# Optimization experiments

Hardware: AMD Instinct MI355X
Metric: run time of the kernel (lower is better)

The kernel has to match this reference:

```python
import jax, jax.numpy as jnp
import numpy as np

WINDOW = 16  # window_size from init_kwargs


def sigmoid_cutoff(x):
    # max(min(1.2*sigmoid(x) - 0.1, 1), 0)
    return jnp.clip(1.2 * jax.nn.sigmoid(x) - 0.1, 0.0, 1.0)


def setup_inputs() -> dict:
    key = jax.random.key(0)
    k1, k2, k3 = jax.random.split(key, 3)
    B, S, H = 8, 2048, 1024
    x = jax.random.normal(k1, (B, S, H), dtype=jnp.float32)
    # Dense kernels (glorot-ish scale), x_layer has no bias, y_layer has bias
    Wx = jax.random.normal(k2, (H, H), dtype=jnp.float32) * (1.0 / np.sqrt(H))
    Wy = jax.random.normal(k3, (H, 2 * H), dtype=jnp.float32) * (1.0 / np.sqrt(H))
    by = jnp.zeros((2 * H,), dtype=jnp.float32)
    return {"x": x, "Wx": Wx, "Wy": Wy, "by": by}


def reference(x, Wx, Wy, by):
    B, S, H = x.shape
    # left-pad sequence with window_size-1 zeros, then project once (x_layer)
    xp = jnp.pad(x, ((0, 0), (WINDOW - 1, 0), (0, 0)))
    proj = jnp.einsum('bsh,hd->bsd', xp, Wx)  # [B, S+W-1, H]

    def step(state, i):
        # inputs[:, i:S+i] in the original loop
        inp = jax.lax.dynamic_slice_in_dim(proj, i, S, axis=1)  # [B,S,H]
        ns = jnp.einsum('bsh,hd->bsd', state, Wy) + by          # [B,S,2H]
        # reshape [B,S,2,H]: channel 0 = candidate, channel 1 = gate
        cand, gate_logits = jnp.split(ns, 2, axis=-1)
        gate = sigmoid_cutoff(gate_logits)
        new_state = jax.nn.relu(gate * (inp + cand) + (1.0 - gate) * state)
        return new_state, None

    state0 = jnp.zeros_like(x)
    state, _ = jax.lax.scan(step, state0, jnp.arange(WINDOW))
    return state
```

## Files before the change

### kernel.cpp

```cpp
#include <hip/hip_runtime.h>

#define H 1024
#define SEQ 2048
#define MROWS 16384
#define KD 1024
#define NTK 16
#define EPW 72

typedef _Float16 f16;
typedef _Float16 f16x8 __attribute__((ext_vector_type(8)));
typedef float f32x4 __attribute__((ext_vector_type(4)));

__device__ __forceinline__ float gate_fn(float x) {
    float s = 1.0f / (1.0f + __expf(-x));
    return fminf(fmaxf(1.2f * s - 0.1f, 0.0f), 1.0f);
}

__device__ __forceinline__ void gload_lds16(const void* g, void* lds) {
    __builtin_amdgcn_global_load_lds(
        (const __attribute__((address_space(1))) unsigned int*)g,
        (__attribute__((address_space(3))) unsigned int*)lds, 16, 0, 0);
}

__global__ void k_f32_to_f16(const float* __restrict__ in, f16* __restrict__ out) {
    size_t i = ((size_t)blockIdx.x * blockDim.x + threadIdx.x) * 8;
    float4 v0 = *(const float4*)(in + i);
    float4 v1 = *(const float4*)(in + i + 4);
    f16x8 o;
    o[0] = (f16)v0.x; o[1] = (f16)v0.y; o[2] = (f16)v0.z; o[3] = (f16)v0.w;
    o[4] = (f16)v1.x; o[5] = (f16)v1.y; o[6] = (f16)v1.z; o[7] = (f16)v1.w;
    *(f16x8*)(out + i) = o;
}

__global__ void k_transpose_f16(const float* __restrict__ Wsrc, f16* __restrict__ WT,
                                int K, int N) {
    __shared__ float tile[32][33];
    int n0 = blockIdx.x * 32, k0 = blockIdx.y * 32;
    for (int i = threadIdx.y; i < 32; i += 8)
        tile[i][threadIdx.x] = Wsrc[(size_t)(k0 + i) * N + n0 + threadIdx.x];
    __syncthreads();
    for (int i = threadIdx.y; i < 32; i += 8)
        WT[(size_t)(n0 + i) * K + k0 + threadIdx.x] = (f16)tile[threadIdx.x][i];
}

__global__ __launch_bounds__(256) void k_proj_gemm(const f16* __restrict__ A,
                                                   const f16* __restrict__ BT,
                                                   f16* __restrict__ P16) {
    __shared__ alignas(16) f16 Alds[128 * 32];
    __shared__ alignas(16) f16 Blds[128 * 32];
    const int tid = threadIdx.x;
    const int lane = tid & 63, wid = tid >> 6;
    const int l15 = lane & 15, l4 = lane >> 4;
    const int bm = blockIdx.x, bn = blockIdx.y;

    const f16* gA[2]; const f16* gB[2];
    char* ldsA[2]; char* ldsB[2];
#pragma unroll
    for (int it = 0; it < 2; ++it) {
        int c = it * 4 + wid;
        int row = c * 16 + (lane >> 2);
        int kch = (lane & 3) ^ ((row >> 1) & 3);
        gA[it] = A + (size_t)(bm * 128 + row) * KD + kch * 8;
        gB[it] = BT + (size_t)(bn * 128 + row) * KD + kch * 8;
        ldsA[it] = (char*)Alds + c * 1024;
        ldsB[it] = (char*)Blds + c * 1024;
    }

    int offA[2], offB[8];
#pragma unroll
    for (int m = 0; m < 2; ++m) {
        int row = wid * 32 + m * 16 + l15;
        offA[m] = row * 64 + ((l4 ^ ((row >> 1) & 3)) << 4);
    }
#pragma unroll
    for (int n = 0; n < 8; ++n) {
        int row = n * 16 + l15;
        offB[n] = row * 64 + ((l4 ^ ((row >> 1) & 3)) << 4);
    }

    f32x4 acc[2][8] = {};

    for (int kt = 0; kt < KD / 32; ++kt) {
        __syncthreads();
#pragma unroll
        for (int it = 0; it < 2; ++it) {
            gload_lds16(gA[it], ldsA[it]);
            gload_lds16(gB[it], ldsB[it]);
            gA[it] += 32; gB[it] += 32;
        }
        __syncthreads();
        f16x8 a[2], b[8];
#pragma unroll
        for (int m = 0; m < 2; ++m) a[m] = *(const f16x8*)((const char*)Alds + offA[m]);
#pragma unroll
        for (int n = 0; n < 8; ++n) b[n] = *(const f16x8*)((const char*)Blds + offB[n]);
#pragma unroll
        for (int n = 0; n < 8; ++n)
#pragma unroll
            for (int m = 0; m < 2; ++m)
                acc[m][n] = __builtin_amdgcn_mfma_f32_16x16x32_f16(a[m], b[n], acc[m][n], 0, 0, 0);
    }

#pragma unroll
    for (int m = 0; m < 2; ++m)
#pragma unroll
        for (int n = 0; n < 8; ++n) {
            int col = bn * 128 + n * 16 + l15;
#pragma unroll
            for (int r = 0; r < 4; ++r) {
                int row = bm * 128 + wid * 32 + m * 16 + l4 * 4 + r;
                P16[(size_t)row * H + col] = (f16)acc[m][n][r];
            }
        }
}

__global__ void k_step0(const f16* __restrict__ P16, const float* __restrict__ by,
                        f16* __restrict__ S16) {
    size_t idx = ((size_t)blockIdx.x * blockDim.x + threadIdx.x) * 8;
    int row = (int)(idx >> 10);
    int d = (int)(idx & 1023);
    int s = row & (SEQ - 1);
    f16x8 p = {};
    if (s >= 15) p = *(const f16x8*)(P16 + (size_t)(row - 15) * H + d);
    float4 byc0 = *(const float4*)(by + d);
    float4 byc1 = *(const float4*)(by + d + 4);
    float4 byg0 = *(const float4*)(by + H + d);
    float4 byg1 = *(const float4*)(by + H + d + 4);
    f16x8 sv;
#pragma unroll
    for (int j = 0; j < 8; ++j) {
        float byc = (j < 4) ? ((const float*)&byc0)[j] : ((const float*)&byc1)[j - 4];
        float byg = (j < 4) ? ((const float*)&byg0)[j] : ((const float*)&byg1)[j - 4];
        float g = gate_fn(byg);
        float v = fmaxf(g * ((float)p[j] + byc), 0.f);
        sv[j] = (f16)v;
    }
    *(f16x8*)(S16 + idx) = sv;
}

__global__ __launch_bounds__(512) void k_step_gemm256(const f16* __restrict__ A,
                                                      const f16* __restrict__ BT,
                                                      const f16* __restrict__ P16,
                                                      const float* __restrict__ by,
                                                      float* __restrict__ Out,
                                                      f16* __restrict__ Snext,
                                                      int stepi) {
    __shared__ alignas(16) char lds[131072];
    const int tid = threadIdx.x;
    const int lane = tid & 63, w = tid >> 6;
    const int l15 = lane & 15, l4 = lane >> 4;
    const int wr = w >> 2, wc = w & 3;

    const int orig = blockIdx.x;
    const int wg = (orig & 7) * 64 + (orig >> 3);
    const int bm = wg >> 3, cbn = wg & 7;

    const int r0 = w * 16 + (lane >> 2), r1 = r0 + 128;
    const int slot = (lane & 3) ^ ((r0 >> 1) & 3);
    const char* pA0 = (const char*)A + ((size_t)(bm * 256 + r0) * KD + slot * 8) * 2;
    const char* pA1 = (const char*)A + ((size_t)(bm * 256 + r1) * KD + slot * 8) * 2;
    const int gB0 = ((r0 >> 5) & 1) * H + cbn * 128 + (r0 >> 6) * 32 + (r0 & 31);
    const int gB1 = ((r1 >> 5) & 1) * H + cbn * 128 + (r1 >> 6) * 32 + (r1 & 31);
    const char* pB0 = (const char*)BT + ((size_t)gB0 * KD + slot * 8) * 2;
    const char* pB1 = (const char*)BT + ((size_t)gB1 * KD + slot * 8) * 2;
    const int dst = w * 1024 + lane * 16;

#define STAGE(bp) do { \
        gload_lds16(pA0,       (bp) + dst); \
        gload_lds16(pA1,       (bp) + 8192 + dst); \
        gload_lds16(pA0 + 64,  (bp) + 16384 + dst); \
        gload_lds16(pA1 + 64,  (bp) + 16384 + 8192 + dst); \
        gload_lds16(pB0,       (bp) + 32768 + dst); \
        gload_lds16(pB1,       (bp) + 32768 + 8192 + dst); \
        gload_lds16(pB0 + 64,  (bp) + 49152 + dst); \
        gload_lds16(pB1 + 64,  (bp) + 49152 + 8192 + dst); \
        pA0 += 128; pA1 += 128; pB0 += 128; pB1 += 128; } while (0)

    const int sx = (l4 ^ ((l15 >> 1) & 3)) << 4;
    int offA[8], offB[4];
#pragma unroll
    for (int m = 0; m < 8; ++m) offA[m] = (wr * 128 + m * 16 + l15) * 64 + sx;
#pragma unroll
    for (int n = 0; n < 4; ++n) offB[n] = 32768 + (wc * 64 + n * 16 + l15) * 64 + sx;

    f32x4 acc[8][4] = {};

    char* cb = lds;
    char* nx = lds + 65536;

    STAGE(cb);
    __syncthreads();

    for (int t = 0; t < NTK; ++t) {
        if (t + 1 < NTK) STAGE(nx);
#pragma unroll
        for (int kh = 0; kh < 2; ++kh) {
            f16x8 a[8], b[4];
#pragma unroll
            for (int m = 0; m < 8; ++m) a[m] = *(const f16x8*)(cb + kh * 16384 + offA[m]);
#pragma unroll
            for (int n = 0; n < 4; ++n) b[n] = *(const f16x8*)(cb + kh * 16384 + offB[n]);
            __builtin_amdgcn_s_setprio(1);
#pragma unroll
            for (int m = 0; m < 8; ++m)
#pragma unroll
                for (int n = 0; n < 4; ++n)
                    acc[m][n] = __builtin_amdgcn_mfma_f32_16x16x32_f16(a[m], b[n], acc[m][n], 0, 0, 0);
            __builtin_amdgcn_s_setprio(0);
        }
        __syncthreads();
        char* tmp = cb; cb = nx; nx = tmp;
    }
#undef STAGE

    const bool last = (stepi == 15);
    f16* Cand = (f16*)lds;
    f16* Gate = (f16*)(lds + 256 * EPW * 2);
#pragma unroll
    for (int rnd = 0; rnd < 2; ++rnd) {
#pragma unroll
        for (int m = 0; m < 8; ++m)
#pragma unroll
            for (int r4 = 0; r4 < 4; ++r4) {
                int row = wr * 128 + m * 16 + l4 * 4 + r4;
                int cr = wc * 16 + l15;
                Cand[row * EPW + cr] = (f16)acc[m][rnd][r4];
                Gate[row * EPW + cr] = (f16)acc[m][rnd + 2][r4];
            }
        __syncthreads();
        const int g = tid & 7;
        const int rb = tid >> 3;
        const int ctile = (g >> 1) * 32 + rnd * 16 + (g & 1) * 8;
        const int d = cbn * 128 + ctile;
        const int cr0 = g * 8;
        float4 byc0 = *(const float4*)(by + d);
        float4 byc1 = *(const float4*)(by + d + 4);
        float4 byg0 = *(const float4*)(by + H + d);
        float4 byg1 = *(const float4*)(by + H + d + 4);
#pragma unroll
        for (int p = 0; p < 4; ++p) {
            int row = p * 64 + rb;
            int grow = bm * 256 + row;
            int s = grow & (SEQ - 1);
            f16x8 c8 = *(const f16x8*)(Cand + row * EPW + cr0);
            f16x8 g8 = *(const f16x8*)(Gate + row * EPW + cr0);
            f16x8 p8 = {};
            if (s >= 15 - stepi)
                p8 = *(const f16x8*)(P16 + (size_t)(grow + stepi - 15) * H + d);
            f16x8 s8 = *(const f16x8*)(A + (size_t)grow * H + d);
            f16x8 o8; float ov[8];
#pragma unroll
            for (int j = 0; j < 8; ++j) {
                float byc = (j < 4) ? ((const float*)&byc0)[j] : ((const float*)&byc1)[j - 4];
                float byg = (j < 4) ? ((const float*)&byg0)[j] : ((const float*)&byg1)[j - 4];
                float cand = (float)c8[j] + byc;
                float gg = gate_fn((float)g8[j] + byg);
                float v = fmaxf(gg * ((float)p8[j] + cand) + (1.f - gg) * (float)s8[j], 0.f);
                o8[j] = (f16)v; ov[j] = v;
            }
            if (!last) {
                *(f16x8*)(Snext + (size_t)grow * H + d) = o8;
            } else {
                *(float4*)(Out + (size_t)grow * H + d) = make_float4(ov[0], ov[1], ov[2], ov[3]);
                *(float4*)(Out + (size_t)grow * H + d + 4) = make_float4(ov[4], ov[5], ov[6], ov[7]);
            }
        }
        __syncthreads();
    }
}

extern "C" void kernel_launch(void* const* d_in, const int* in_sizes, int n_in,
                              void* d_out, int out_size, void* d_ws, size_t ws_size,
                              hipStream_t stream) {
    (void)in_sizes; (void)n_in; (void)out_size; (void)ws_size;
    const float* x  = (const float*)d_in[0];
    const float* Wx = (const float*)d_in[1];
    const float* Wy = (const float*)d_in[2];
    const float* by = (const float*)d_in[3];
    float* out = (float*)d_out;

    char* ws = (char*)d_ws;
    const size_t MB = 1024ull * 1024ull;
    f16* st16a = (f16*)(ws);
    f16* st16b = (f16*)(ws + 32 * MB);
    f16* P16   = (f16*)(ws + 64 * MB);
    f16* WxT   = (f16*)(ws + 96 * MB);
    f16* WyT   = (f16*)(ws + 98 * MB);

    hipLaunchKernelGGL(k_f32_to_f16, dim3(MROWS * H / 8 / 256), dim3(256), 0, stream, x, st16a);
    hipLaunchKernelGGL(k_transpose_f16, dim3(H / 32, H / 32), dim3(32, 8), 0, stream, Wx, WxT, H, H);
    hipLaunchKernelGGL(k_transpose_f16, dim3(2 * H / 32, H / 32), dim3(32, 8), 0, stream, Wy, WyT, H, 2 * H);
    hipLaunchKernelGGL(k_proj_gemm, dim3(MROWS / 128, H / 128), dim3(256), 0, stream, st16a, WxT, P16);
    hipLaunchKernelGGL(k_step0, dim3(MROWS * H / 8 / 256), dim3(256), 0, stream, P16, by, st16b);

    f16* bufs[2] = {st16a, st16b};
    for (int i = 1; i <= 15; ++i) {
        const f16* cur = bufs[i & 1];
        f16* nxt = bufs[(i + 1) & 1];
        hipLaunchKernelGGL(k_step_gemm256, dim3(MROWS / 256 * 8), dim3(512), 0, stream,
                           cur, WyT, P16, by, out, nxt, i);
    }
}
```

Before: 1.320 ms.

## Shrink step GEMM tile to 256x128 with K=32 stages for higher occupancy

Changes the per-step recurrent GEMM from a 256x256 output tile (128 KB LDS, K=64 stages) to a 256x128 tile (64 candidate plus 64 gate columns) with K=32 stages and 72 KB LDS. The launch doubles the grid and sets launch_bounds(512,4) to allow more waves resident per CU. The aim is better latency hiding and more even load across CUs. The cost is lower arithmetic intensity per tile, more A-matrix rereads, and twice as many barrier iterations per K loop.

```diff
diff --git a/kernel.cpp b/kernel.cpp
--- a/kernel.cpp
+++ b/kernel.cpp
@@ -4,7 +4,7 @@
 #define SEQ 2048
 #define MROWS 16384
 #define KD 1024
-#define NTK 16
+#define NT32 32
 #define EPW 72
 
 typedef _Float16 f16;
@@ -138,76 +138,68 @@
     *(f16x8*)(S16 + idx) = sv;
 }
 
-__global__ __launch_bounds__(512) void k_step_gemm256(const f16* __restrict__ A,
+__global__ __launch_bounds__(512, 4) void k_step_gemm(const f16* __restrict__ A,
                                                       const f16* __restrict__ BT,
                                                       const f16* __restrict__ P16,
                                                       const float* __restrict__ by,
                                                       float* __restrict__ Out,
                                                       f16* __restrict__ Snext,
                                                       int stepi) {
-    __shared__ alignas(16) char lds[131072];
+    __shared__ alignas(16) char lds[73728];
     const int tid = threadIdx.x;
     const int lane = tid & 63, w = tid >> 6;
     const int l15 = lane & 15, l4 = lane >> 4;
-    const int wr = w >> 2, wc = w & 3;
+    const int wr = w >> 1, wc = w & 1;
 
     const int orig = blockIdx.x;
-    const int wg = (orig & 7) * 64 + (orig >> 3);
-    const int bm = wg >> 3, cbn = wg & 7;
-
-    const int r0 = w * 16 + (lane >> 2), r1 = r0 + 128;
-    const int slot = (lane & 3) ^ ((r0 >> 1) & 3);
-    const char* pA0 = (const char*)A + ((size_t)(bm * 256 + r0) * KD + slot * 8) * 2;
-    const char* pA1 = (const char*)A + ((size_t)(bm * 256 + r1) * KD + slot * 8) * 2;
-    const int gB0 = ((r0 >> 5) & 1) * H + cbn * 128 + (r0 >> 6) * 32 + (r0 & 31);
-    const int gB1 = ((r1 >> 5) & 1) * H + cbn * 128 + (r1 >> 6) * 32 + (r1 & 31);
-    const char* pB0 = (const char*)BT + ((size_t)gB0 * KD + slot * 8) * 2;
-    const char* pB1 = (const char*)BT + ((size_t)gB1 * KD + slot * 8) * 2;
+    const int wg = (orig & 7) * 128 + (orig >> 3);
+    const int bm = wg >> 4, tb = wg & 15;
+
+    const int rA0 = w * 16 + (lane >> 2), rA1 = rA0 + 128;
+    const int slotA = (lane & 3) ^ ((rA0 >> 1) & 3);
+    const char* pA0 = (const char*)A + ((size_t)(bm * 256 + rA0) * KD + slotA * 8) * 2;
+    const char* pA1 = (const char*)A + ((size_t)(bm * 256 + rA1) * KD + slotA * 8) * 2;
+    const int rB = rA0;
+    const int rowB = ((rB & 32) ? H : 0) + tb * 64 + ((rB >> 6) << 5) + (rB & 31);
+    const int slotB = (lane & 3) ^ ((rB >> 1) & 3);
+    const char* pB = (const char*)BT + ((size_t)rowB * KD + slotB * 8) * 2;
     const int dst = w * 1024 + lane * 16;
 
 #define STAGE(bp) do { \
-        gload_lds16(pA0,       (bp) + dst); \
-        gload_lds16(pA1,       (bp) + 8192 + dst); \
-        gload_lds16(pA0 + 64,  (bp) + 16384 + dst); \
-        gload_lds16(pA1 + 64,  (bp) + 16384 + 8192 + dst); \
-        gload_lds16(pB0,       (bp) + 32768 + dst); \
-        gload_lds16(pB1,       (bp) + 32768 + 8192 + dst); \
-        gload_lds16(pB0 + 64,  (bp) + 49152 + dst); \
-        gload_lds16(pB1 + 64,  (bp) + 49152 + 8192 + dst); \
-        pA0 += 128; pA1 += 128; pB0 += 128; pB1 += 128; } while (0)
+        gload_lds16(pA0, (bp) + dst); \
+        gload_lds16(pA1, (bp) + 8192 + dst); \
+        gload_lds16(pB,  (bp) + 16384 + dst); \
+        pA0 += 64; pA1 += 64; pB += 64; } while (0)
 
     const int sx = (l4 ^ ((l15 >> 1) & 3)) << 4;
-    int offA[8], offB[4];
-#pragma unroll
-    for (int m = 0; m < 8; ++m) offA[m] = (wr * 128 + m * 16 + l15) * 64 + sx;
-#pragma unroll
-    for (int n = 0; n < 4; ++n) offB[n] = 32768 + (wc * 64 + n * 16 + l15) * 64 + sx;
-
-    f32x4 acc[8][4] = {};
+    int offA[4], offB[4];
+#pragma unroll
+    for (int m = 0; m < 4; ++m) offA[m] = (wr * 64 + m * 16 + l15) * 64 + sx;
+#pragma unroll
+    for (int n = 0; n < 4; ++n) offB[n] = 16384 + (wc * 64 + n * 16 + l15) * 64 + sx;
+
+    f32x4 acc[4][4] = {};
 
     char* cb = lds;
-    char* nx = lds + 65536;
+    char* nx = lds + 24576;
 
     STAGE(cb);
     __syncthreads();
 
-    for (int t = 0; t < NTK; ++t) {
-        if (t + 1 < NTK) STAGE(nx);
-#pragma unroll
-        for (int kh = 0; kh < 2; ++kh) {
-            f16x8 a[8], b[4];
-#pragma unroll
-            for (int m = 0; m < 8; ++m) a[m] = *(const f16x8*)(cb + kh * 16384 + offA[m]);
-#pragma unroll
-            for (int n = 0; n < 4; ++n) b[n] = *(const f16x8*)(cb + kh * 16384 + offB[n]);
-            __builtin_amdgcn_s_setprio(1);
-#pragma unroll
-            for (int m = 0; m < 8; ++m)
-#pragma unroll
-                for (int n = 0; n < 4; ++n)
-                    acc[m][n] = __builtin_amdgcn_mfma_f32_16x16x32_f16(a[m], b[n], acc[m][n], 0, 0, 0);
-            __builtin_amdgcn_s_setprio(0);
-        }
+    for (int t = 0; t < NT32; ++t) {
+        if (t + 1 < NT32) STAGE(nx);
+        f16x8 a[4], b[4];
+#pragma unroll
+        for (int m = 0; m < 4; ++m) a[m] = *(const f16x8*)(cb + offA[m]);
+#pragma unroll
+        for (int n = 0; n < 4; ++n) b[n] = *(const f16x8*)(cb + offB[n]);
+        __builtin_amdgcn_s_setprio(1);
+#pragma unroll
+        for (int m = 0; m < 4; ++m)
+#pragma unroll
+            for (int n = 0; n < 4; ++n)
+                acc[m][n] = __builtin_amdgcn_mfma_f32_16x16x32_f16(a[m], b[n], acc[m][n], 0, 0, 0);
+        __builtin_amdgcn_s_setprio(0);
         __syncthreads();
         char* tmp = cb; cb = nx; nx = tmp;
     }
@@ -215,24 +207,24 @@
 
     const bool last = (stepi == 15);
     f16* Cand = (f16*)lds;
-    f16* Gate = (f16*)(lds + 256 * EPW * 2);
-#pragma unroll
-    for (int rnd = 0; rnd < 2; ++rnd) {
-#pragma unroll
-        for (int m = 0; m < 8; ++m)
+    f16* Gate = (f16*)(lds + 36864);
+#pragma unroll
+    for (int m = 0; m < 4; ++m)
+#pragma unroll
+        for (int n = 0; n < 2; ++n)
 #pragma unroll
             for (int r4 = 0; r4 < 4; ++r4) {
-                int row = wr * 128 + m * 16 + l4 * 4 + r4;
-                int cr = wc * 16 + l15;
-                Cand[row * EPW + cr] = (f16)acc[m][rnd][r4];
-                Gate[row * EPW + cr] = (f16)acc[m][rnd + 2][r4];
-            }
-        __syncthreads();
+                int row = wr * 64 + m * 16 + l4 * 4 + r4;
+                int cc = wc * 32 + n * 16 + l15;
+                Cand[row * EPW + cc] = (f16)acc[m][n][r4];
+                Gate[row * EPW + cc] = (f16)acc[m][n + 2][r4];
+            }
+    __syncthreads();
+    {
         const int g = tid & 7;
         const int rb = tid >> 3;
-        const int ctile = (g >> 1) * 32 + rnd * 16 + (g & 1) * 8;
-        const int d = cbn * 128 + ctile;
-        const int cr0 = g * 8;
+        const int dl = g * 8;
+        const int d = tb * 64 + dl;
         float4 byc0 = *(const float4*)(by + d);
         float4 byc1 = *(const float4*)(by + d + 4);
         float4 byg0 = *(const float4*)(by + H + d);
@@ -242,8 +234,8 @@
             int row = p * 64 + rb;
             int grow = bm * 256 + row;
             int s = grow & (SEQ - 1);
-            f16x8 c8 = *(const f16x8*)(Cand + row * EPW + cr0);
-            f16x8 g8 = *(const f16x8*)(Gate + row * EPW + cr0);
+            f16x8 c8 = *(const f16x8*)(Cand + row * EPW + dl);
+            f16x8 g8 = *(const f16x8*)(Gate + row * EPW + dl);
             f16x8 p8 = {};
             if (s >= 15 - stepi)
                 p8 = *(const f16x8*)(P16 + (size_t)(grow + stepi - 15) * H + d);
@@ -265,7 +257,6 @@
                 *(float4*)(Out + (size_t)grow * H + d + 4) = make_float4(ov[4], ov[5], ov[6], ov[7]);
             }
         }
-        __syncthreads();
     }
 }
 
@@ -297,7 +288,7 @@
     for (int i = 1; i <= 15; ++i) {
         const f16* cur = bufs[i & 1];
         f16* nxt = bufs[(i + 1) & 1];
-        hipLaunchKernelGGL(k_step_gemm256, dim3(MROWS / 256 * 8), dim3(512), 0, stream,
+        hipLaunchKernelGGL(k_step_gemm, dim3(MROWS / 256 * 16), dim3(512), 0, stream,
                            cur, WyT, P16, by, out, nxt, i);
     }
 }
```

Result: faster. 1.286 ms (-2.6%).
